# Optimization experiments

Hardware: AMD Instinct MI355X
Metric: run time of the kernel (lower is better)

The kernel has to match this reference:

```python
import jax, jax.numpy as jnp
import numpy as np

N = 100_000   # nodes
E = 1_600_000 # edges
F = 64        # in_feats
H = 64        # hid
EPS = 1e-5


def setup_inputs() -> dict:
    key = jax.random.key(0)
    ks = jax.random.split(key, 12)
    s = 1.0 / np.sqrt(F)
    inp = {
        "x":   jax.random.normal(ks[0], (N, F), jnp.float32),
        "src": jax.random.randint(ks[1], (E,), 0, N, jnp.int32),
        "dst": jax.random.randint(ks[2], (E,), 0, N, jnp.int32),
        # GraphConv 1: in_feats -> hid
        "W1": jax.random.uniform(ks[3], (F, H), jnp.float32, -s, s),
        "b1": jnp.zeros((H,), jnp.float32),
        "g1": jnp.ones((H,), jnp.float32),
        "be1": jnp.zeros((H,), jnp.float32),
        # GraphConv 2: hid -> hid
        "W2": jax.random.uniform(ks[4], (H, H), jnp.float32, -s, s),
        "b2": jnp.zeros((H,), jnp.float32),
        "g2": jnp.ones((H,), jnp.float32),
        "be2": jnp.zeros((H,), jnp.float32),
        # classifier hid -> 2
        "Wc": jax.random.uniform(ks[5], (H, 2), jnp.float32, -s, s),
        "bc": jnp.zeros((2,), jnp.float32),
    }
    return inp


def _graph_conv(x, src, dst, W, b):
    # DGL GraphConv, norm='both', allow_zero_in_degree=True:
    # h = D_in^{-1/2} A (D_out^{-1/2} x) W + b, degrees clamped to >= 1.
    n = x.shape[0]
    ones = jnp.ones(src.shape[0], x.dtype)
    deg_out = jnp.clip(jax.ops.segment_sum(ones, src, num_segments=n), 1.0)
    deg_in = jnp.clip(jax.ops.segment_sum(ones, dst, num_segments=n), 1.0)
    h = x * jax.lax.rsqrt(deg_out)[:, None]
    m = jax.ops.segment_sum(h[src], dst, num_segments=n)  # gather-scatter SpMM
    m = m * jax.lax.rsqrt(deg_in)[:, None]
    return m @ W + b


def _bn(h, g, be):
    # BatchNorm1d training-mode math over nodes (biased variance).
    mu = h.mean(axis=0)
    var = h.var(axis=0)
    return (h - mu) * jax.lax.rsqrt(var + EPS) * g + be


def reference(x, src, dst, W1, b1, g1, be1, W2, b2, g2, be2, Wc, bc):
    h = jax.nn.relu(_bn(_graph_conv(x, src, dst, W1, b1), g1, be1))
    # dropout is identity in eval mode
    h = jax.nn.relu(_bn(_graph_conv(h, src, dst, W2, b2), g2, be2))
    hg = h.mean(axis=0, keepdims=True)  # [1, H] graph readout
    return hg @ Wc + bc                 # [1, 2]
```

## Files before the change

kernel.cpp:

```cpp
#include <hip/hip_runtime.h>
#include <hip/hip_fp16.h>

#define FDIM 64
#define EPS 1e-5f
#define NBUCK 1024
#define LOWB 7
#define LOWMASK 127
#define RB 256
#define RT 1024
#define GRP 16
#define NSLOT 8

typedef float v2f __attribute__((ext_vector_type(2)));

__global__ void k_hist(const int* __restrict__ src, const int* __restrict__ dst,
                       int* __restrict__ histS, int* __restrict__ histD, int E, int chunk) {
    __shared__ int hs[NBUCK], hd[NBUCK];
    int tid = threadIdx.x;
    hs[tid] = 0; hd[tid] = 0;
    __syncthreads();
    int b = blockIdx.x;
    int beg = b * chunk;
    int end = min(E, beg + chunk);
    int i = beg + tid * 4;
    for (; i + 3 < end; i += RT * 4) {
        int4 s = *(const int4*)(src + i);
        int4 d = *(const int4*)(dst + i);
        atomicAdd(&hs[s.x >> LOWB], 1); atomicAdd(&hd[d.x >> LOWB], 1);
        atomicAdd(&hs[s.y >> LOWB], 1); atomicAdd(&hd[d.y >> LOWB], 1);
        atomicAdd(&hs[s.z >> LOWB], 1); atomicAdd(&hd[d.z >> LOWB], 1);
        atomicAdd(&hs[s.w >> LOWB], 1); atomicAdd(&hd[d.w >> LOWB], 1);
    }
    if (i < end) {
        for (int j = i; j < end && j < i + 4; ++j) {
            atomicAdd(&hs[src[j] >> LOWB], 1);
            atomicAdd(&hd[dst[j] >> LOWB], 1);
        }
    }
    __syncthreads();
    histS[b * NBUCK + tid] = hs[tid];
    histD[b * NBUCK + tid] = hd[tid];
}

__global__ void k_scanA(const int* __restrict__ histS, const int* __restrict__ histD,
                        int* __restrict__ psumS, int* __restrict__ psumD) {
    int bid = blockIdx.x;
    int m = bid >> 6;
    int g = (bid >> 2) & (RB / GRP - 1);
    int c = bid & 3;
    const int* hist = m ? histD : histS;
    int* psum = m ? psumD : psumS;
    int k = c * 256 + threadIdx.x;
    int s = 0;
#pragma unroll
    for (int r = 0; r < GRP; ++r)
        s += hist[(g * GRP + r) * NBUCK + k];
    psum[g * NBUCK + k] = s;
}

__global__ void k_scanB(const int* __restrict__ psumS, int* __restrict__ baseS,
                        int* __restrict__ grpbaseS,
                        const int* __restrict__ psumD, int* __restrict__ baseD,
                        int* __restrict__ grpbaseD) {
    const int* psum = blockIdx.x ? psumD : psumS;
    int* base    = blockIdx.x ? baseD : baseS;
    int* grpbase = blockIdx.x ? grpbaseD : grpbaseS;
    __shared__ int s[NBUCK];
    int k = threadIdx.x;
    int ge[RB / GRP];
    int run = 0;
#pragma unroll
    for (int g = 0; g < RB / GRP; ++g) { ge[g] = run; run += psum[g * NBUCK + k]; }
    s[k] = run;
    __syncthreads();
    for (int off = 1; off < NBUCK; off <<= 1) {
        int t = (k >= off) ? s[k - off] : 0;
        __syncthreads();
        s[k] += t;
        __syncthreads();
    }
    int excl = (k > 0) ? s[k - 1] : 0;
    base[k] = excl;
    if (k == NBUCK - 1) base[NBUCK] = s[NBUCK - 1];
#pragma unroll
    for (int g = 0; g < RB / GRP; ++g)
        grpbase[g * NBUCK + k] = excl + ge[g];
}

__global__ void k_bucket(const int* __restrict__ src, const int* __restrict__ dst,
                         const int* __restrict__ histS, const int* __restrict__ histD,
                         const int* __restrict__ grpbaseS, const int* __restrict__ grpbaseD,
                         unsigned char* __restrict__ tmpS, int* __restrict__ tmpD,
                         int E, int chunk) {
    __shared__ int curS[NBUCK], curD[NBUCK];
    int tid = threadIdx.x;
    int b = blockIdx.x;
    int g = b / GRP;
    int rs = 0, rd = 0;
    for (int r = g * GRP; r < b; ++r) {
        rs += histS[r * NBUCK + tid];
        rd += histD[r * NBUCK + tid];
    }
    curS[tid] = grpbaseS[g * NBUCK + tid] + rs;
    curD[tid] = grpbaseD[g * NBUCK + tid] + rd;
    __syncthreads();
    int beg = b * chunk;
    int end = min(E, beg + chunk);
    int i = beg + tid * 4;
    for (; i + 3 < end; i += RT * 4) {
        int4 s = *(const int4*)(src + i);
        int4 d = *(const int4*)(dst + i);
        int p;
        p = atomicAdd(&curS[s.x >> LOWB], 1); tmpS[p] = (unsigned char)(s.x & LOWMASK);
        p = atomicAdd(&curS[s.y >> LOWB], 1); tmpS[p] = (unsigned char)(s.y & LOWMASK);
        p = atomicAdd(&curS[s.z >> LOWB], 1); tmpS[p] = (unsigned char)(s.z & LOWMASK);
        p = atomicAdd(&curS[s.w >> LOWB], 1); tmpS[p] = (unsigned char)(s.w & LOWMASK);
        p = atomicAdd(&curD[d.x >> LOWB], 1); tmpD[p] = (s.x << LOWB) | (d.x & LOWMASK);
        p = atomicAdd(&curD[d.y >> LOWB], 1); tmpD[p] = (s.y << LOWB) | (d.y & LOWMASK);
        p = atomicAdd(&curD[d.z >> LOWB], 1); tmpD[p] = (s.z << LOWB) | (d.z & LOWMASK);
        p = atomicAdd(&curD[d.w >> LOWB], 1); tmpD[p] = (s.w << LOWB) | (d.w & LOWMASK);
    }
    if (i < end) {
        for (int j = i; j < end && j < i + 4; ++j) {
            int sv = src[j], dv = dst[j];
            int p = atomicAdd(&curS[sv >> LOWB], 1);
            tmpS[p] = (unsigned char)(sv & LOWMASK);
            p = atomicAdd(&curD[dv >> LOWB], 1);
            tmpD[p] = (sv << LOWB) | (dv & LOWMASK);
        }
    }
}

__global__ void k_fine(const int* __restrict__ tmpD, const int* __restrict__ baseD,
                       int* __restrict__ csr_src, int* __restrict__ rowptr,
                       const unsigned char* __restrict__ tmpS, const int* __restrict__ baseS,
                       int* __restrict__ degO, const float* __restrict__ x,
                       unsigned char* __restrict__ buf8, int N, int nbuck) {
    __shared__ int hist[128];
    __shared__ int scanv[128];
    int tid = threadIdx.x;
    if (blockIdx.x < nbuck) {
        int b = blockIdx.x;
        int s0 = baseD[b];
        int s1 = baseD[b + 1];
        if (tid < 128) hist[tid] = 0;
        __syncthreads();
        for (int i = s0 + tid; i < s1; i += 256)
            atomicAdd(&hist[tmpD[i] & LOWMASK], 1);
        __syncthreads();
        int mine = (tid < 128) ? hist[tid] : 0;
        if (tid < 128) scanv[tid] = mine;
        __syncthreads();
        for (int off = 1; off < 128; off <<= 1) {
            int t = (tid < 128 && tid >= off) ? scanv[tid - off] : 0;
            __syncthreads();
            if (tid < 128) scanv[tid] += t;
            __syncthreads();
        }
        if (tid < 128) {
            int excl = scanv[tid] - mine;
            int d = (b << LOWB) + tid;
            if (d <= N) rowptr[d] = s0 + excl;
            hist[tid] = excl;
        }
        __syncthreads();
        for (int i = s0 + tid; i < s1; i += 256) {
            int p = tmpD[i];
            int pos = atomicAdd(&hist[p & LOWMASK], 1);
            csr_src[s0 + pos] = p >> LOWB;
        }
    } else {
        int b = blockIdx.x - nbuck;
        int s0 = baseS[b];
        int s1 = baseS[b + 1];
        if (tid < 128) hist[tid] = 0;
        __syncthreads();
        for (int i = s0 + tid; i < s1; i += 256)
            atomicAdd(&hist[tmpS[i]], 1);
        __syncthreads();
        if (tid < 128) {
            int d = (b << LOWB) + tid;
            if (d < N) degO[d] = hist[tid];
        }
        int node = (b << LOWB) + (tid >> 1);
        if (node < N) {
            float rs = rsqrtf((float)max(hist[tid >> 1], 1));
            int part = tid & 1;
            const float4* xr = (const float4*)(x + (size_t)node * FDIM) + part * 8;
            int4* orow = (int4*)(buf8 + (size_t)node * FDIM + part * 32);
            int wbuf[8];
#pragma unroll
            for (int q = 0; q < 4; ++q) {
                float4 a = xr[2 * q];
                float4 c = xr[2 * q + 1];
                int t = __builtin_amdgcn_cvt_pk_fp8_f32(a.x * rs, a.y * rs, 0, false);
                t     = __builtin_amdgcn_cvt_pk_fp8_f32(a.z * rs, a.w * rs, t, true);
                wbuf[2 * q] = t;
                t = __builtin_amdgcn_cvt_pk_fp8_f32(c.x * rs, c.y * rs, 0, false);
                t = __builtin_amdgcn_cvt_pk_fp8_f32(c.z * rs, c.w * rs, t, true);
                wbuf[2 * q + 1] = t;
            }
            orow[0] = make_int4(wbuf[0], wbuf[1], wbuf[2], wbuf[3]);
            orow[1] = make_int4(wbuf[4], wbuf[5], wbuf[6], wbuf[7]);
        }
    }
}

__global__ void k_spmm8(const unsigned char* __restrict__ hin, const int* __restrict__ rowptr,
                        const int* __restrict__ csr_src, __half* __restrict__ out, int N) {
    int wid = (blockIdx.x * blockDim.x + threadIdx.x) >> 6;
    int lane = threadIdx.x & 63;
    int g  = lane >> 3;
    int sl = lane & 7;
    int e  = (lane >> 2) & 1;
    int s  = lane & 3;
    int row = wid * 8 + g;
    bool rv = row < N;
    int start = rv ? rowptr[row] : 0;
    int end   = rv ? rowptr[row + 1] : 0;
    int deg = end - start;
    int md = deg;
    md = max(md, __shfl_xor(md, 8));
    md = max(md, __shfl_xor(md, 16));
    md = max(md, __shfl_xor(md, 32));
    float acc[16];
#pragma unroll
    for (int q = 0; q < 16; ++q) acc[q] = 0.f;
    int safe = (deg > 0) ? end - 1 : 0;
    int a0 = start + sl;
    int idx_cur = csr_src[(a0 < end) ? a0 : safe];
    for (int it = 0; it < md; it += 8) {
        int idx_nxt = 0;
        if (it + 8 < md) {
            int a = start + it + 8 + sl;
            idx_nxt = csr_src[(a < end) ? a : safe];
        }
        int b0 = __shfl(idx_cur, (g << 3) + e);
        int b1 = __shfl(idx_cur, (g << 3) + e + 2);
        int b2 = __shfl(idx_cur, (g << 3) + e + 4);
        int b3 = __shfl(idx_cur, (g << 3) + e + 6);
        uint4 r0 = ((const uint4*)(hin + ((size_t)b0 << 6)))[s];
        uint4 r1 = ((const uint4*)(hin + ((size_t)b1 << 6)))[s];
        uint4 r2 = ((const uint4*)(hin + ((size_t)b2 << 6)))[s];
        uint4 r3 = ((const uint4*)(hin + ((size_t)b3 << 6)))[s];
        __builtin_amdgcn_sched_barrier(0);
        float w0 = (it + e     < deg) ? 1.f : 0.f;
        float w1 = (it + e + 2 < deg) ? 1.f : 0.f;
        float w2 = (it + e + 4 < deg) ? 1.f : 0.f;
        float w3 = (it + e + 6 < deg) ? 1.f : 0.f;
#define ACC16(RV, W) do { \
        v2f t0 = __builtin_amdgcn_cvt_pk_f32_fp8((int)RV.x, false); \
        v2f t1 = __builtin_amdgcn_cvt_pk_f32_fp8((int)RV.x, true);  \
        v2f t2 = __builtin_amdgcn_cvt_pk_f32_fp8((int)RV.y, false); \
        v2f t3 = __builtin_amdgcn_cvt_pk_f32_fp8((int)RV.y, true);  \
        v2f t4 = __builtin_amdgcn_cvt_pk_f32_fp8((int)RV.z, false); \
        v2f t5 = __builtin_amdgcn_cvt_pk_f32_fp8((int)RV.z, true);  \
        v2f t6 = __builtin_amdgcn_cvt_pk_f32_fp8((int)RV.w, false); \
        v2f t7 = __builtin_amdgcn_cvt_pk_f32_fp8((int)RV.w, true);  \
        acc[0]  = fmaf(W, t0.x, acc[0]);  acc[1]  = fmaf(W, t0.y, acc[1]);  \
        acc[2]  = fmaf(W, t1.x, acc[2]);  acc[3]  = fmaf(W, t1.y, acc[3]);  \
        acc[4]  = fmaf(W, t2.x, acc[4]);  acc[5]  = fmaf(W, t2.y, acc[5]);  \
        acc[6]  = fmaf(W, t3.x, acc[6]);  acc[7]  = fmaf(W, t3.y, acc[7]);  \
        acc[8]  = fmaf(W, t4.x, acc[8]);  acc[9]  = fmaf(W, t4.y, acc[9]);  \
        acc[10] = fmaf(W, t5.x, acc[10]); acc[11] = fmaf(W, t5.y, acc[11]); \
        acc[12] = fmaf(W, t6.x, acc[12]); acc[13] = fmaf(W, t6.y, acc[13]); \
        acc[14] = fmaf(W, t7.x, acc[14]); acc[15] = fmaf(W, t7.y, acc[15]); \
    } while (0)
        ACC16(r0, w0);
        ACC16(r1, w1);
        ACC16(r2, w2);
        ACC16(r3, w3);
#undef ACC16
        idx_cur = idx_nxt;
    }
#pragma unroll
    for (int q = 0; q < 16; ++q) acc[q] += __shfl_xor(acc[q], 4);
    if (rv) {
        float rs = rsqrtf(fmaxf((float)deg, 1.0f));
        float v0 = e ? acc[8]  : acc[0];
        float v1 = e ? acc[9]  : acc[1];
        float v2 = e ? acc[10] : acc[2];
        float v3 = e ? acc[11] : acc[3];
        float v4 = e ? acc[12] : acc[4];
        float v5 = e ? acc[13] : acc[5];
        float v6 = e ? acc[14] : acc[6];
        float v7 = e ? acc[15] : acc[7];
        union { float4 f; __half2 h[4]; } o;
        o.h[0] = __floats2half2_rn(v0 * rs, v1 * rs);
        o.h[1] = __floats2half2_rn(v2 * rs, v3 * rs);
        o.h[2] = __floats2half2_rn(v4 * rs, v5 * rs);
        o.h[3] = __floats2half2_rn(v6 * rs, v7 * rs);
        *(float4*)(out + ((size_t)row << 6) + (s << 4) + (e << 3)) = o.f;
    }
}

__global__ void k_gemm_reg(const __half* __restrict__ m, const float* __restrict__ W,
                           const float* __restrict__ b, __half* __restrict__ out, int N) {
    int n = blockIdx.x * blockDim.x + threadIdx.x;
    if (n >= N) return;
    const __half2* mrow = (const __half2*)(m + (size_t)n * FDIM);
    float acc[FDIM];
#pragma unroll
    for (int j = 0; j < FDIM; ++j) acc[j] = b[j];
    for (int k0 = 0; k0 < FDIM; k0 += 8) {
        float2 f0 = __half22float2(mrow[(k0 >> 1) + 0]);
        float2 f1 = __half22float2(mrow[(k0 >> 1) + 1]);
        float2 f2 = __half22float2(mrow[(k0 >> 1) + 2]);
        float2 f3 = __half22float2(mrow[(k0 >> 1) + 3]);
        float mreg[8] = {f0.x, f0.y, f1.x, f1.y, f2.x, f2.y, f3.x, f3.y};
#pragma unroll
        for (int k1 = 0; k1 < 8; ++k1) {
            const float* Wrow = W + (k0 + k1) * FDIM;
#pragma unroll
            for (int j = 0; j < FDIM; ++j)
                acc[j] = fmaf(mreg[k1], Wrow[j], acc[j]);
        }
    }
    float4* orow = (float4*)(out + (size_t)n * FDIM);
#pragma unroll
    for (int j = 0; j < FDIM; j += 8) {
        union { __half2 h[4]; float4 f; } u;
        u.h[0] = __floats2half2_rn(acc[j + 0], acc[j + 1]);
        u.h[1] = __floats2half2_rn(acc[j + 2], acc[j + 3]);
        u.h[2] = __floats2half2_rn(acc[j + 4], acc[j + 5]);
        u.h[3] = __floats2half2_rn(acc[j + 6], acc[j + 7]);
        orow[j >> 3] = u.f;
    }
}

__global__ void k_stats_fin(const __half* __restrict__ h, float* __restrict__ ssum,
                            float* __restrict__ ssq, const float* __restrict__ g,
                            float* __restrict__ mu, float* __restrict__ coef,
                            int* __restrict__ cnt, int N) {
    __shared__ float red[4][128];
    __shared__ int lastv;
    int tid = threadIdx.x;
    int sl = tid & 7;
    int nl = tid >> 3;
    float s[8] = {0.f,0.f,0.f,0.f,0.f,0.f,0.f,0.f};
    float q[8] = {0.f,0.f,0.f,0.f,0.f,0.f,0.f,0.f};
    int stride = gridDim.x * 32;
    for (int n = blockIdx.x * 32 + nl; n < N; n += stride) {
        union { float4 f; __half2 hh[4]; } u;
        u.f = ((const float4*)(h + ((size_t)n << 6)))[sl];
#pragma unroll
        for (int p = 0; p < 4; ++p) {
            float2 v = __half22float2(u.hh[p]);
            s[2*p]   += v.x; q[2*p]   += v.x * v.x;
            s[2*p+1] += v.y; q[2*p+1] += v.y * v.y;
        }
    }
#pragma unroll
    for (int off = 8; off < 64; off <<= 1) {
#pragma unroll
        for (int p = 0; p < 8; ++p) {
            s[p] += __shfl_xor(s[p], off);
            q[p] += __shfl_xor(q[p], off);
        }
    }
    int wv = tid >> 6, lane = tid & 63;
    if (lane < 8) {
#pragma unroll
        for (int p = 0; p < 8; ++p) {
            red[wv][lane * 8 + p] = s[p];
            red[wv][64 + lane * 8 + p] = q[p];
        }
    }
    __syncthreads();
    int slot = (blockIdx.x & (NSLOT - 1)) << 6;
    if (tid < 128) {
        float v = red[0][tid] + red[1][tid] + red[2][tid] + red[3][tid];
        if (tid < 64) atomicAdd(&ssum[slot + tid], v);
        else          atomicAdd(&ssq[slot + tid - 64], v);
    }
    __syncthreads();
    if (tid == 0)
        lastv = (__hip_atomic_fetch_add(cnt, 1, __ATOMIC_ACQ_REL,
                                        __HIP_MEMORY_SCOPE_AGENT) == (int)gridDim.x - 1);
    __syncthreads();
    if (lastv && tid < 64) {
        float sv = 0.f, qv = 0.f;
#pragma unroll
        for (int p = 0; p < NSLOT; ++p) {
            sv += __hip_atomic_load(&ssum[(p << 6) + tid], __ATOMIC_RELAXED,
                                    __HIP_MEMORY_SCOPE_AGENT);
            qv += __hip_atomic_load(&ssq[(p << 6) + tid], __ATOMIC_RELAXED,
                                    __HIP_MEMORY_SCOPE_AGENT);
        }
        float m = sv / (float)N;
        float var = qv / (float)N - m * m;
        mu[tid] = m;
        coef[tid] = rsqrtf(var + EPS) * g[tid];
    }
}

__global__ void k_bnrelu_scale(const float2* __restrict__ h, const float* __restrict__ mu,
                               const float* __restrict__ coef, const float* __restrict__ be,
                               const int* __restrict__ degO, int* __restrict__ out8, int n4) {
    int i = blockIdx.x * blockDim.x + threadIdx.x;
    if (i < n4) {
        int n = i >> 4;
        int j4 = (i & 15) << 2;
        float rs = rsqrtf((float)max(degO[n], 1));
        union { __half2 hh[2]; float2 f; } u;
        u.f = h[i];
        float2 v0 = __half22float2(u.hh[0]);
        float2 v1 = __half22float2(u.hh[1]);
        float r0 = fmaxf((v0.x - mu[j4 + 0]) * coef[j4 + 0] + be[j4 + 0], 0.f) * rs;
        float r1 = fmaxf((v0.y - mu[j4 + 1]) * coef[j4 + 1] + be[j4 + 1], 0.f) * rs;
        float r2 = fmaxf((v1.x - mu[j4 + 2]) * coef[j4 + 2] + be[j4 + 2], 0.f) * rs;
        float r3 = fmaxf((v1.y - mu[j4 + 3]) * coef[j4 + 3] + be[j4 + 3], 0.f) * rs;
        int wv = __builtin_amdgcn_cvt_pk_fp8_f32(r0, r1, 0, false);
        wv     = __builtin_amdgcn_cvt_pk_fp8_f32(r2, r3, wv, true);
        out8[i] = wv;
    }
}

__global__ void k_bnmean_fin(const __half* __restrict__ h, const float* __restrict__ mu,
                             const float* __restrict__ coef, const float* __restrict__ be,
                             float* __restrict__ hsum, const float* __restrict__ Wc,
                             const float* __restrict__ bc, float* __restrict__ out,
                             int* __restrict__ cnt, int N) {
    __shared__ float red[4][64];
    __shared__ float cls[128];
    __shared__ int lastv;
    int tid = threadIdx.x;
    int sl = tid & 7;
    int nl = tid >> 3;
    int j8 = sl * 8;
    float m_[8], c_[8], b_[8];
#pragma unroll
    for (int p = 0; p < 8; ++p) { m_[p] = mu[j8 + p]; c_[p] = coef[j8 + p]; b_[p] = be[j8 + p]; }
    float s[8] = {0.f,0.f,0.f,0.f,0.f,0.f,0.f,0.f};
    int stride = gridDim.x * 32;
    for (int n = blockIdx.x * 32 + nl; n < N; n += stride) {
        union { float4 f; __half2 hh[4]; } u;
        u.f = ((const float4*)(h + ((size_t)n << 6)))[sl];
#pragma unroll
        for (int p = 0; p < 4; ++p) {
            float2 v = __half22float2(u.hh[p]);
            s[2*p]   += fmaxf((v.x - m_[2*p])   * c_[2*p]   + b_[2*p],   0.f);
            s[2*p+1] += fmaxf((v.y - m_[2*p+1]) * c_[2*p+1] + b_[2*p+1], 0.f);
        }
    }
#pragma unroll
    for (int off = 8; off < 64; off <<= 1) {
#pragma unroll
        for (int p = 0; p < 8; ++p) s[p] += __shfl_xor(s[p], off);
    }
    int wv = tid >> 6, lane = tid & 63;
    if (lane < 8) {
#pragma unroll
        for (int p = 0; p < 8; ++p) red[wv][lane * 8 + p] = s[p];
    }
    __syncthreads();
    int slot = (blockIdx.x & (NSLOT - 1)) << 6;
    if (tid < 64)
        atomicAdd(&hsum[slot + tid], red[0][tid] + red[1][tid] + red[2][tid] + red[3][tid]);
    __syncthreads();
    if (tid == 0)
        lastv = (__hip_atomic_fetch_add(cnt, 1, __ATOMIC_ACQ_REL,
                                        __HIP_MEMORY_SCOPE_AGENT) == (int)gridDim.x - 1);
    __syncthreads();
    if (lastv) {
        if (tid < 64) {
            float hg = 0.f;
#pragma unroll
            for (int p = 0; p < NSLOT; ++p)
                hg += __hip_atomic_load(&hsum[(p << 6) + tid], __ATOMIC_RELAXED,
                                        __HIP_MEMORY_SCOPE_AGENT);
            hg /= (float)N;
            cls[tid]      = hg * Wc[tid * 2 + 0];
            cls[64 + tid] = hg * Wc[tid * 2 + 1];
        }
        __syncthreads();
        if (tid == 0) {
            float a = 0.f, bv = 0.f;
            for (int k = 0; k < 64; ++k) { a += cls[k]; bv += cls[64 + k]; }
            out[0] = a + bc[0];
            out[1] = bv + bc[1];
        }
    }
}

extern "C" void kernel_launch(void* const* d_in, const int* in_sizes, int n_in,
                              void* d_out, int out_size, void* d_ws, size_t ws_size,
                              hipStream_t stream) {
    const float* x   = (const float*)d_in[0];
    const int*   src = (const int*)d_in[1];
    const int*   dst = (const int*)d_in[2];
    const float* W1  = (const float*)d_in[3];
    const float* b1  = (const float*)d_in[4];
    const float* g1  = (const float*)d_in[5];
    const float* be1 = (const float*)d_in[6];
    const float* W2  = (const float*)d_in[7];
    const float* b2  = (const float*)d_in[8];
    const float* g2  = (const float*)d_in[9];
    const float* be2 = (const float*)d_in[10];
    const float* Wc  = (const float*)d_in[11];
    const float* bc  = (const float*)d_in[12];
    float* out = (float*)d_out;

    const int N = in_sizes[0] / FDIM;
    const int E = in_sizes[1];

    char* w = (char*)d_ws;
    __half* bufA   = (__half*)w;
    __half* bufB   = bufA + (size_t)N * FDIM;
    int*   csr_src = (int*)(bufB + (size_t)N * FDIM);
    int*   degO    = csr_src + E;
    int*   rowptr  = degO + N;
    int*   histS   = rowptr + N + 2;
    int*   histD   = histS + RB * NBUCK;
    int*   baseS   = histD + RB * NBUCK;
    int*   baseD   = baseS + NBUCK + 1;
    int*   psumS   = baseD + NBUCK + 1;
    int*   psumD   = psumS + (RB / GRP) * NBUCK;
    int*   grpbaseS= psumD + (RB / GRP) * NBUCK;
    int*   grpbaseD= grpbaseS + (RB / GRP) * NBUCK;
    float* stats   = (float*)(grpbaseD + (RB / GRP) * NBUCK);
    unsigned char* tmpS = (unsigned char*)(stats + 4096);
    unsigned char* buf8 = tmpS + E;
    int*           tmpD = (int*)bufB;

    float* sum1  = stats + 0;
    float* sq1   = stats + 512;
    float* sum2  = stats + 1024;
    float* sq2   = stats + 1536;
    float* hsum  = stats + 2048;
    float* mu1   = stats + 2560;
    float* coef1 = stats + 2624;
    float* mu2   = stats + 2688;
    float* coef2 = stats + 2752;
    int*   cnt1  = (int*)(stats + 2816);
    int*   cnt2  = (int*)(stats + 2817);
    int*   cnt3  = (int*)(stats + 2818);

    const int n4 = N * (FDIM / 4);
    const int spmm8_blocks = ((N + 7) / 8 + 3) / 4;
    const int nbuck_active = (N + LOWMASK) >> LOWB;
    const int chunk = ((E + RB - 1) / RB + 3) & ~3;

    hipMemsetAsync(stats, 0, 4096 * 4, stream);

    k_hist<<<RB, RT, 0, stream>>>(src, dst, histS, histD, E, chunk);
    k_scanA<<<2 * (RB / GRP) * 4, 256, 0, stream>>>(histS, histD, psumS, psumD);
    k_scanB<<<2, NBUCK, 0, stream>>>(psumS, baseS, grpbaseS, psumD, baseD, grpbaseD);
    k_bucket<<<RB, RT, 0, stream>>>(src, dst, histS, histD, grpbaseS, grpbaseD,
                                    tmpS, tmpD, E, chunk);
    k_fine<<<2 * nbuck_active, 256, 0, stream>>>(tmpD, baseD, csr_src, rowptr,
                                                 tmpS, baseS, degO, x, buf8, N, nbuck_active);

    k_spmm8<<<spmm8_blocks, 256, 0, stream>>>(buf8, rowptr, csr_src, bufB, N);
    k_gemm_reg<<<(N + 63) / 64, 64, 0, stream>>>(bufB, W1, b1, bufA, N);
    k_stats_fin<<<256, 256, 0, stream>>>(bufA, sum1, sq1, g1, mu1, coef1, cnt1, N);
    k_bnrelu_scale<<<(n4 + 255) / 256, 256, 0, stream>>>((const float2*)bufA, mu1, coef1, be1,
                                                         degO, (int*)buf8, n4);
    k_spmm8<<<spmm8_blocks, 256, 0, stream>>>(buf8, rowptr, csr_src, bufB, N);
    k_gemm_reg<<<(N + 63) / 64, 64, 0, stream>>>(bufB, W2, b2, bufA, N);
    k_stats_fin<<<256, 256, 0, stream>>>(bufA, sum2, sq2, g2, mu2, coef2, cnt2, N);
    k_bnmean_fin<<<256, 256, 0, stream>>>(bufA, mu2, coef2, be2, hsum, Wc, bc, out, cnt3, N);
}
```

Measured before the change: 280.1 us.

## Compute out-degrees with global atomics instead of source-side bucket sort

Out-degrees were previously obtained by radix-bucketing source ids (histogram, scan, scatter of byte-sized low bits, per-bucket fine histogram). That pipeline is replaced by a memset plus one kernel doing global atomicAdd per edge into degO, and the source half is removed from hist/scan/bucket. The aim is to drop one full scatter pass and the extra histogram traffic. It adds 1.6M global atomics over 100K addresses, which may contend more than the shared-memory approach.

```diff
diff --git a/kernel.cpp b/kernel.cpp
--- a/kernel.cpp
+++ b/kernel.cpp
@@ -13,64 +13,63 @@
 
 typedef float v2f __attribute__((ext_vector_type(2)));
 
-__global__ void k_hist(const int* __restrict__ src, const int* __restrict__ dst,
-                       int* __restrict__ histS, int* __restrict__ histD, int E, int chunk) {
-    __shared__ int hs[NBUCK], hd[NBUCK];
+__global__ void k_deg(const int* __restrict__ src, int* __restrict__ degO, int E) {
+    int i = (blockIdx.x * blockDim.x + threadIdx.x) * 4;
+    if (i + 3 < E) {
+        int4 s = *(const int4*)(src + i);
+        atomicAdd(&degO[s.x], 1);
+        atomicAdd(&degO[s.y], 1);
+        atomicAdd(&degO[s.z], 1);
+        atomicAdd(&degO[s.w], 1);
+    } else {
+        for (int j = i; j < E && j < i + 4; ++j)
+            atomicAdd(&degO[src[j]], 1);
+    }
+}
+
+__global__ void k_hist(const int* __restrict__ dst, int* __restrict__ histD, int E, int chunk) {
+    __shared__ int hd[NBUCK];
     int tid = threadIdx.x;
-    hs[tid] = 0; hd[tid] = 0;
+    hd[tid] = 0;
     __syncthreads();
     int b = blockIdx.x;
     int beg = b * chunk;
     int end = min(E, beg + chunk);
     int i = beg + tid * 4;
     for (; i + 3 < end; i += RT * 4) {
-        int4 s = *(const int4*)(src + i);
         int4 d = *(const int4*)(dst + i);
-        atomicAdd(&hs[s.x >> LOWB], 1); atomicAdd(&hd[d.x >> LOWB], 1);
-        atomicAdd(&hs[s.y >> LOWB], 1); atomicAdd(&hd[d.y >> LOWB], 1);
-        atomicAdd(&hs[s.z >> LOWB], 1); atomicAdd(&hd[d.z >> LOWB], 1);
-        atomicAdd(&hs[s.w >> LOWB], 1); atomicAdd(&hd[d.w >> LOWB], 1);
+        atomicAdd(&hd[d.x >> LOWB], 1);
+        atomicAdd(&hd[d.y >> LOWB], 1);
+        atomicAdd(&hd[d.z >> LOWB], 1);
+        atomicAdd(&hd[d.w >> LOWB], 1);
     }
     if (i < end) {
-        for (int j = i; j < end && j < i + 4; ++j) {
-            atomicAdd(&hs[src[j] >> LOWB], 1);
+        for (int j = i; j < end && j < i + 4; ++j)
             atomicAdd(&hd[dst[j] >> LOWB], 1);
-        }
-    }
-    __syncthreads();
-    histS[b * NBUCK + tid] = hs[tid];
+    }
+    __syncthreads();
     histD[b * NBUCK + tid] = hd[tid];
 }
 
-__global__ void k_scanA(const int* __restrict__ histS, const int* __restrict__ histD,
-                        int* __restrict__ psumS, int* __restrict__ psumD) {
-    int bid = blockIdx.x;
-    int m = bid >> 6;
-    int g = (bid >> 2) & (RB / GRP - 1);
-    int c = bid & 3;
-    const int* hist = m ? histD : histS;
-    int* psum = m ? psumD : psumS;
+__global__ void k_scanA(const int* __restrict__ histD, int* __restrict__ psumD) {
+    int g = blockIdx.x >> 2;
+    int c = blockIdx.x & 3;
     int k = c * 256 + threadIdx.x;
     int s = 0;
 #pragma unroll
     for (int r = 0; r < GRP; ++r)
-        s += hist[(g * GRP + r) * NBUCK + k];
-    psum[g * NBUCK + k] = s;
-}
-
-__global__ void k_scanB(const int* __restrict__ psumS, int* __restrict__ baseS,
-                        int* __restrict__ grpbaseS,
-                        const int* __restrict__ psumD, int* __restrict__ baseD,
+        s += histD[(g * GRP + r) * NBUCK + k];
+    psumD[g * NBUCK + k] = s;
+}
+
+__global__ void k_scanB(const int* __restrict__ psumD, int* __restrict__ baseD,
                         int* __restrict__ grpbaseD) {
-    const int* psum = blockIdx.x ? psumD : psumS;
-    int* base    = blockIdx.x ? baseD : baseS;
-    int* grpbase = blockIdx.x ? grpbaseD : grpbaseS;
     __shared__ int s[NBUCK];
     int k = threadIdx.x;
     int ge[RB / GRP];
     int run = 0;
 #pragma unroll
-    for (int g = 0; g < RB / GRP; ++g) { ge[g] = run; run += psum[g * NBUCK + k]; }
+    for (int g = 0; g < RB / GRP; ++g) { ge[g] = run; run += psumD[g * NBUCK + k]; }
     s[k] = run;
     __syncthreads();
     for (int off = 1; off < NBUCK; off <<= 1) {
@@ -80,28 +79,23 @@
         __syncthreads();
     }
     int excl = (k > 0) ? s[k - 1] : 0;
-    base[k] = excl;
-    if (k == NBUCK - 1) base[NBUCK] = s[NBUCK - 1];
+    baseD[k] = excl;
+    if (k == NBUCK - 1) baseD[NBUCK] = s[NBUCK - 1];
 #pragma unroll
     for (int g = 0; g < RB / GRP; ++g)
-        grpbase[g * NBUCK + k] = excl + ge[g];
+        grpbaseD[g * NBUCK + k] = excl + ge[g];
 }
 
 __global__ void k_bucket(const int* __restrict__ src, const int* __restrict__ dst,
-                         const int* __restrict__ histS, const int* __restrict__ histD,
-                         const int* __restrict__ grpbaseS, const int* __restrict__ grpbaseD,
-                         unsigned char* __restrict__ tmpS, int* __restrict__ tmpD,
-                         int E, int chunk) {
-    __shared__ int curS[NBUCK], curD[NBUCK];
+                         const int* __restrict__ histD, const int* __restrict__ grpbaseD,
+                         int* __restrict__ tmpD, int E, int chunk) {
+    __shared__ int curD[NBUCK];
     int tid = threadIdx.x;
     int b = blockIdx.x;
     int g = b / GRP;
-    int rs = 0, rd = 0;
-    for (int r = g * GRP; r < b; ++r) {
-        rs += histS[r * NBUCK + tid];
+    int rd = 0;
+    for (int r = g * GRP; r < b; ++r)
         rd += histD[r * NBUCK + tid];
-    }
-    curS[tid] = grpbaseS[g * NBUCK + tid] + rs;
     curD[tid] = grpbaseD[g * NBUCK + tid] + rd;
     __syncthreads();
     int beg = b * chunk;
@@ -111,10 +105,6 @@
         int4 s = *(const int4*)(src + i);
         int4 d = *(const int4*)(dst + i);
         int p;
-        p = atomicAdd(&curS[s.x >> LOWB], 1); tmpS[p] = (unsigned char)(s.x & LOWMASK);
-        p = atomicAdd(&curS[s.y >> LOWB], 1); tmpS[p] = (unsigned char)(s.y & LOWMASK);
-        p = atomicAdd(&curS[s.z >> LOWB], 1); tmpS[p] = (unsigned char)(s.z & LOWMASK);
-        p = atomicAdd(&curS[s.w >> LOWB], 1); tmpS[p] = (unsigned char)(s.w & LOWMASK);
         p = atomicAdd(&curD[d.x >> LOWB], 1); tmpD[p] = (s.x << LOWB) | (d.x & LOWMASK);
         p = atomicAdd(&curD[d.y >> LOWB], 1); tmpD[p] = (s.y << LOWB) | (d.y & LOWMASK);
         p = atomicAdd(&curD[d.z >> LOWB], 1); tmpD[p] = (s.z << LOWB) | (d.z & LOWMASK);
@@ -123,9 +113,7 @@
     if (i < end) {
         for (int j = i; j < end && j < i + 4; ++j) {
             int sv = src[j], dv = dst[j];
-            int p = atomicAdd(&curS[sv >> LOWB], 1);
-            tmpS[p] = (unsigned char)(sv & LOWMASK);
-            p = atomicAdd(&curD[dv >> LOWB], 1);
+            int p = atomicAdd(&curD[dv >> LOWB], 1);
             tmpD[p] = (sv << LOWB) | (dv & LOWMASK);
         }
     }
@@ -133,8 +121,7 @@
 
 __global__ void k_fine(const int* __restrict__ tmpD, const int* __restrict__ baseD,
                        int* __restrict__ csr_src, int* __restrict__ rowptr,
-                       const unsigned char* __restrict__ tmpS, const int* __restrict__ baseS,
-                       int* __restrict__ degO, const float* __restrict__ x,
+                       const int* __restrict__ degO, const float* __restrict__ x,
                        unsigned char* __restrict__ buf8, int N, int nbuck) {
     __shared__ int hist[128];
     __shared__ int scanv[128];
@@ -171,20 +158,9 @@
         }
     } else {
         int b = blockIdx.x - nbuck;
-        int s0 = baseS[b];
-        int s1 = baseS[b + 1];
-        if (tid < 128) hist[tid] = 0;
-        __syncthreads();
-        for (int i = s0 + tid; i < s1; i += 256)
-            atomicAdd(&hist[tmpS[i]], 1);
-        __syncthreads();
-        if (tid < 128) {
-            int d = (b << LOWB) + tid;
-            if (d < N) degO[d] = hist[tid];
-        }
         int node = (b << LOWB) + (tid >> 1);
         if (node < N) {
-            float rs = rsqrtf((float)max(hist[tid >> 1], 1));
+            float rs = rsqrtf((float)max(degO[node], 1));
             int part = tid & 1;
             const float4* xr = (const float4*)(x + (size_t)node * FDIM) + part * 8;
             int4* orow = (int4*)(buf8 + (size_t)node * FDIM + part * 32);
@@ -510,17 +486,12 @@
     int*   csr_src = (int*)(bufB + (size_t)N * FDIM);
     int*   degO    = csr_src + E;
     int*   rowptr  = degO + N;
-    int*   histS   = rowptr + N + 2;
-    int*   histD   = histS + RB * NBUCK;
-    int*   baseS   = histD + RB * NBUCK;
-    int*   baseD   = baseS + NBUCK + 1;
-    int*   psumS   = baseD + NBUCK + 1;
-    int*   psumD   = psumS + (RB / GRP) * NBUCK;
-    int*   grpbaseS= psumD + (RB / GRP) * NBUCK;
-    int*   grpbaseD= grpbaseS + (RB / GRP) * NBUCK;
+    int*   histD   = rowptr + N + 2;
+    int*   baseD   = histD + RB * NBUCK;
+    int*   psumD   = baseD + NBUCK + 1;
+    int*   grpbaseD= psumD + (RB / GRP) * NBUCK;
     float* stats   = (float*)(grpbaseD + (RB / GRP) * NBUCK);
-    unsigned char* tmpS = (unsigned char*)(stats + 4096);
-    unsigned char* buf8 = tmpS + E;
+    unsigned char* buf8 = (unsigned char*)(stats + 4096);
     int*           tmpD = (int*)bufB;
 
     float* sum1  = stats + 0;
@@ -540,16 +511,18 @@
     const int spmm8_blocks = ((N + 7) / 8 + 3) / 4;
     const int nbuck_active = (N + LOWMASK) >> LOWB;
     const int chunk = ((E + RB - 1) / RB + 3) & ~3;
+    const int deg_blocks = ((E + 3) / 4 + 255) / 256;
 
     hipMemsetAsync(stats, 0, 4096 * 4, stream);
-
-    k_hist<<<RB, RT, 0, stream>>>(src, dst, histS, histD, E, chunk);
-    k_scanA<<<2 * (RB / GRP) * 4, 256, 0, stream>>>(histS, histD, psumS, psumD);
-    k_scanB<<<2, NBUCK, 0, stream>>>(psumS, baseS, grpbaseS, psumD, baseD, grpbaseD);
-    k_bucket<<<RB, RT, 0, stream>>>(src, dst, histS, histD, grpbaseS, grpbaseD,
-                                    tmpS, tmpD, E, chunk);
+    hipMemsetAsync(degO, 0, (size_t)N * 4, stream);
+
+    k_deg<<<deg_blocks, 256, 0, stream>>>(src, degO, E);
+    k_hist<<<RB, RT, 0, stream>>>(dst, histD, E, chunk);
+    k_scanA<<<(RB / GRP) * 4, 256, 0, stream>>>(histD, psumD);
+    k_scanB<<<1, NBUCK, 0, stream>>>(psumD, baseD, grpbaseD);
+    k_bucket<<<RB, RT, 0, stream>>>(src, dst, histD, grpbaseD, tmpD, E, chunk);
     k_fine<<<2 * nbuck_active, 256, 0, stream>>>(tmpD, baseD, csr_src, rowptr,
-                                                 tmpS, baseS, degO, x, buf8, N, nbuck_active);
+                                                 degO, x, buf8, N, nbuck_active);
 
     k_spmm8<<<spmm8_blocks, 256, 0, stream>>>(buf8, rowptr, csr_src, bufB, N);
     k_gemm_reg<<<(N + 63) / 64, 64, 0, stream>>>(bufB, W1, b1, bufA, N);
```

Result: slower. 335.6 us (+19.8%).
